# Kernel optimization log

Hardware: AMD Instinct MI355X
Metric: run time of the kernel (lower is better)

Reference implementation:

```python
import jax, jax.numpy as jnp
import numpy as np

B, C, H, W = 512, 1, 280, 280
K, S, F = 28, 28, 10           # kernel, stride, nfilters
HS, WS = 10, 10                # output spatial spans (280/28)
SPAN = HS * WS                 # 100 patch locations
OUT = 10                       # out_channels
DEC_IN = HS * WS * F           # 1000


def setup_inputs() -> dict:
    key = jax.random.key(0)
    k1, k2, k3, k4, k5 = jax.random.split(key, 5)
    x = jax.random.normal(k1, (B, C, H, W), dtype=jnp.float32)
    # locally-connected weights: one kernel per (filter, spatial location), torch layout [F*SPAN, C, K, K]
    conv_w = jax.random.normal(k2, (F * SPAN, C, K, K), dtype=jnp.float32) * 0.02
    conv_b = jax.random.normal(k3, (F * SPAN, C), dtype=jnp.float32) * 0.02
    dec_w = jax.random.normal(k4, (OUT, DEC_IN), dtype=jnp.float32) * 0.02
    dec_b = jax.random.normal(k5, (OUT,), dtype=jnp.float32) * 0.02
    return {"x": x, "conv_w": conv_w, "conv_b": conv_b, "dec_w": dec_w, "dec_b": dec_b}


def reference(x, conv_w, conv_b, dec_w, dec_b):
    # Extract non-overlapping KxK patches (stride == kernel_size, padding == 0):
    # [B,C,H,W] -> [B,C,HS,K,WS,K] -> [B,HS,WS,C,K,K] -> [B,SPAN,C,K,K]
    # matches torch unfold(2).unfold(3) ordering (height span outer, width span inner).
    patches = x.reshape(B, C, HS, K, WS, K).transpose(0, 2, 4, 1, 3, 5)
    patches = patches.reshape(B, SPAN, C, K, K)
    # weight index in torch is f*SPAN + s (x is tiled SPAN-fastest by repeat)
    w = conv_w.reshape(F, SPAN, C, K, K)
    # per-location elementwise mul + reduce over (kh, kw) == batched tiny contraction
    out = jnp.einsum('bscij,fscij->bfsc', patches, w)  # [B,F,SPAN,C]
    out = out + conv_b.reshape(F, SPAN, C)
    out = out.reshape(B, F, HS, WS)  # valid since C == 1 (as in torch view)
    out = jax.nn.relu(out).reshape(B, DEC_IN)
    return out @ dec_w.T + dec_b
```

## Files before the change

### kernel.cpp

```cpp
#include <hip/hip_runtime.h>

#define HW      280
#define IMG     78400
#define KK      28
#define F_N     10
#define SPAN    100
#define OUT_N   10
#define NB      4
#define RQR     14
#define WQ      (RQR * 7)
#define P_PLANE 512000

__device__ __forceinline__ float red8(float v) {
  v += __int_as_float(__builtin_amdgcn_mov_dpp(__float_as_int(v), 0xB1, 0xF, 0xF, true));
  v += __int_as_float(__builtin_amdgcn_mov_dpp(__float_as_int(v), 0x4E, 0xF, 0xF, true));
  v += __int_as_float(__builtin_amdgcn_ds_swizzle(__float_as_int(v), 0x101F));
  return v;
}

__global__ __launch_bounds__(256) void lcn_conv(
    const float* __restrict__ x, const float* __restrict__ cw,
    float* __restrict__ P) {
  const int bid = blockIdx.x;
  const int t   = bid & 7;
  const int s   = bid >> 3;
  const int rq  = t >> 2;
  const int bg  = t & 3;
  const int hs  = s / 10, ws = s - hs * 10;

  const int lane = threadIdx.x & 63;
  const int wid  = threadIdx.x >> 6;
  const int c4   = lane & 7;
  const int g    = lane >> 3;
  const int b0   = bg * 128 + wid * 32 + g * 4;

  __shared__ float4 wl[F_N * WQ];
  {
    const float4* wg = reinterpret_cast<const float4*>(cw);
    for (int i = (int)threadIdx.x; i < F_N * WQ; i += 256) {
      const int f = i / WQ, rem = i - f * WQ;
      wl[i] = wg[(f * SPAN + s) * 196 + rq * WQ + rem];
    }
  }
  __syncthreads();

  float acc[NB][F_N];
#pragma unroll
  for (int bi = 0; bi < NB; ++bi)
#pragma unroll
    for (int f = 0; f < F_N; ++f) acc[bi][f] = 0.f;

  const float* xb = x + (size_t)(hs * KK + rq * RQR) * HW + ws * KK + c4 * 4;
  const float* xr[NB];
#pragma unroll
  for (int bi = 0; bi < NB; ++bi) xr[bi] = xb + (size_t)(b0 + bi) * IMG;

#define COMPUTE(ROW, XV)                                                  \
  {                                                                       \
    _Pragma("unroll")                                                     \
    for (int f = 0; f < F_N; ++f) {                                       \
      const float4 wv = wl[f * WQ + (ROW) * 7 + c4];                      \
      _Pragma("unroll")                                                   \
      for (int bi = 0; bi < NB; ++bi) {                                   \
        acc[bi][f] = fmaf(XV[bi].x, wv.x, acc[bi][f]);                    \
        acc[bi][f] = fmaf(XV[bi].y, wv.y, acc[bi][f]);                    \
        acc[bi][f] = fmaf(XV[bi].z, wv.z, acc[bi][f]);                    \
        acc[bi][f] = fmaf(XV[bi].w, wv.w, acc[bi][f]);                    \
      }                                                                   \
    }                                                                     \
  }

  if (c4 < 7) {
    float4 xvA[NB], xvB[NB];
#pragma unroll
    for (int bi = 0; bi < NB; ++bi)
      xvA[bi] = *reinterpret_cast<const float4*>(xr[bi]);
    for (int r = 0; r < RQR; r += 2) {
#pragma unroll
      for (int bi = 0; bi < NB; ++bi)
        xvB[bi] = *reinterpret_cast<const float4*>(xr[bi] + (size_t)(r + 1) * HW);
      COMPUTE(r, xvA)
      if (r + 2 < RQR) {
#pragma unroll
        for (int bi = 0; bi < NB; ++bi)
          xvA[bi] = *reinterpret_cast<const float4*>(xr[bi] + (size_t)(r + 2) * HW);
      }
      COMPUTE(r + 1, xvB)
    }
  }

#pragma unroll
  for (int bi = 0; bi < NB; ++bi)
#pragma unroll
    for (int f = 0; f < F_N; ++f) acc[bi][f] = red8(acc[bi][f]);

  float* Pp = P + (size_t)rq * P_PLANE + (size_t)s * 512 + b0;
#pragma unroll
  for (int f = 0; f < F_N; ++f) {
    if (c4 == f || c4 == f - 8) {
#pragma unroll
      for (int bi = 0; bi < NB; ++bi)
        Pp[(size_t)f * (SPAN * 512) + bi] = acc[bi][f];
    }
  }
}

__global__ __launch_bounds__(256) void lcn_dec(
    const float* __restrict__ P, const float* __restrict__ cb,
    const float* __restrict__ dw, float* __restrict__ yp) {
  const int bid    = blockIdx.x;
  const int dchunk = bid >> 3;
  const int bg     = bid & 7;
  const int lane   = threadIdx.x & 63;
  const int swid   = __builtin_amdgcn_readfirstlane((int)(threadIdx.x >> 6));
  const int d0     = dchunk * 40 + swid * 10;

  const float* Pb = P + (size_t)bg * 64 + lane;
  float acc[OUT_N];
#pragma unroll
  for (int o = 0; o < OUT_N; ++o) acc[o] = 0.f;

#pragma unroll
  for (int dd = 0; dd < 10; ++dd) {
    const int d = d0 + dd;
    const float p = Pb[(size_t)d * 512] + Pb[(size_t)d * 512 + P_PLANE];
    const float h = fmaxf(p + cb[d], 0.f);
#pragma unroll
    for (int o = 0; o < OUT_N; ++o)
      acc[o] = fmaf(h, dw[o * 1000 + d], acc[o]);
  }
  float* ypp = yp + (size_t)(dchunk * 4 + swid) * 5120 + bg * 64 + lane;
#pragma unroll
  for (int o = 0; o < OUT_N; ++o) ypp[(size_t)o * 512] = acc[o];
}

__global__ __launch_bounds__(256) void lcn_yred(
    const float* __restrict__ yp, const float* __restrict__ db,
    float* __restrict__ y) {
  const int idx = blockIdx.x * 256 + (int)threadIdx.x;
  const int o = idx >> 9;
  const int b = idx & 511;
  float a = db[o];
#pragma unroll 10
  for (int p = 0; p < 100; ++p) a += yp[(size_t)p * 5120 + idx];
  y[b * OUT_N + o] = a;
}

extern "C" void kernel_launch(void* const* d_in, const int* in_sizes, int n_in,
                              void* d_out, int out_size, void* d_ws, size_t ws_size,
                              hipStream_t stream) {
  const float* x  = (const float*)d_in[0];
  const float* cw = (const float*)d_in[1];
  const float* cb = (const float*)d_in[2];
  const float* dw = (const float*)d_in[3];
  const float* db = (const float*)d_in[4];
  float* y = (float*)d_out;

  float* P  = (float*)d_ws;
  float* yp = P + 2 * P_PLANE;

  lcn_conv<<<dim3(800), dim3(256), 0, stream>>>(x, cw, P);
  lcn_dec <<<dim3(200), dim3(256), 0, stream>>>(P, cb, dw, yp);
  lcn_yred<<<dim3(20),  dim3(256), 0, stream>>>(yp, db, y);
}
```

Baseline: 46.84 us.

## Split conv rows into quarters with XCD-aware block mapping and triple-buffered loads

```diff
diff --git a/kernel.cpp b/kernel.cpp
--- a/kernel.cpp
+++ b/kernel.cpp
@@ -7,26 +7,30 @@
 #define SPAN    100
 #define OUT_N   10
 #define NB      4
-#define RQR     14
+#define RQR     7
 #define WQ      (RQR * 7)
 #define P_PLANE 512000
 
 __device__ __forceinline__ float red8(float v) {
-  v += __int_as_float(__builtin_amdgcn_mov_dpp(__float_as_int(v), 0xB1, 0xF, 0xF, true));
-  v += __int_as_float(__builtin_amdgcn_mov_dpp(__float_as_int(v), 0x4E, 0xF, 0xF, true));
-  v += __int_as_float(__builtin_amdgcn_ds_swizzle(__float_as_int(v), 0x101F));
+  v += __int_as_float(__builtin_amdgcn_mov_dpp(__float_as_int(v), 0xB1,  0xF, 0xF, true));
+  v += __int_as_float(__builtin_amdgcn_mov_dpp(__float_as_int(v), 0x4E,  0xF, 0xF, true));
+  v += __int_as_float(__builtin_amdgcn_mov_dpp(__float_as_int(v), 0x141, 0xF, 0xF, true));
   return v;
 }
 
-__global__ __launch_bounds__(256) void lcn_conv(
+__global__ __launch_bounds__(256, 4) void lcn_conv(
     const float* __restrict__ x, const float* __restrict__ cw,
     float* __restrict__ P) {
   const int bid = blockIdx.x;
-  const int t   = bid & 7;
-  const int s   = bid >> 3;
+  const int xcd = bid & 7;
+  const int idx = bid >> 3;
+  const int ws  = idx % 10;
+  const int u   = xcd * 20 + idx / 10;
+  const int hs  = u % 10;
+  const int t   = u / 10;
   const int rq  = t >> 2;
   const int bg  = t & 3;
-  const int hs  = s / 10, ws = s - hs * 10;
+  const int s   = hs * 10 + ws;
 
   const int lane = threadIdx.x & 63;
   const int wid  = threadIdx.x >> 6;
@@ -51,41 +55,37 @@
     for (int f = 0; f < F_N; ++f) acc[bi][f] = 0.f;
 
   const float* xb = x + (size_t)(hs * KK + rq * RQR) * HW + ws * KK + c4 * 4;
-  const float* xr[NB];
-#pragma unroll
-  for (int bi = 0; bi < NB; ++bi) xr[bi] = xb + (size_t)(b0 + bi) * IMG;
 
-#define COMPUTE(ROW, XV)                                                  \
+#define LOADROW(SLOT, ROW)                                                \
+  _Pragma("unroll")                                                       \
+  for (int bi = 0; bi < NB; ++bi)                                         \
+    xv[SLOT][bi] = *reinterpret_cast<const float4*>(                      \
+        xb + (size_t)(b0 + bi) * IMG + (size_t)(ROW) * HW);
+
+#define COMPUTE(ROW, SLOT)                                                \
   {                                                                       \
     _Pragma("unroll")                                                     \
     for (int f = 0; f < F_N; ++f) {                                       \
       const float4 wv = wl[f * WQ + (ROW) * 7 + c4];                      \
       _Pragma("unroll")                                                   \
       for (int bi = 0; bi < NB; ++bi) {                                   \
-        acc[bi][f] = fmaf(XV[bi].x, wv.x, acc[bi][f]);                    \
-        acc[bi][f] = fmaf(XV[bi].y, wv.y, acc[bi][f]);                    \
-        acc[bi][f] = fmaf(XV[bi].z, wv.z, acc[bi][f]);                    \
-        acc[bi][f] = fmaf(XV[bi].w, wv.w, acc[bi][f]);                    \
+        acc[bi][f] = fmaf(xv[SLOT][bi].x, wv.x, acc[bi][f]);              \
+        acc[bi][f] = fmaf(xv[SLOT][bi].y, wv.y, acc[bi][f]);              \
+        acc[bi][f] = fmaf(xv[SLOT][bi].z, wv.z, acc[bi][f]);              \
+        acc[bi][f] = fmaf(xv[SLOT][bi].w, wv.w, acc[bi][f]);              \
       }                                                                   \
     }                                                                     \
   }
 
   if (c4 < 7) {
-    float4 xvA[NB], xvB[NB];
+    float4 xv[3][NB];
+    LOADROW(0, 0)
+    LOADROW(1, 1)
 #pragma unroll
-    for (int bi = 0; bi < NB; ++bi)
-      xvA[bi] = *reinterpret_cast<const float4*>(xr[bi]);
-    for (int r = 0; r < RQR; r += 2) {
-#pragma unroll
-      for (int bi = 0; bi < NB; ++bi)
-        xvB[bi] = *reinterpret_cast<const float4*>(xr[bi] + (size_t)(r + 1) * HW);
-      COMPUTE(r, xvA)
-      if (r + 2 < RQR) {
-#pragma unroll
-        for (int bi = 0; bi < NB; ++bi)
-          xvA[bi] = *reinterpret_cast<const float4*>(xr[bi] + (size_t)(r + 2) * HW);
-      }
-      COMPUTE(r + 1, xvB)
+    for (int r = 0; r < RQR; ++r) {
+      const int slot = r % 3;
+      if (r + 2 < RQR) { const int ns = (r + 2) % 3; LOADROW(ns, r + 2) }
+      COMPUTE(r, slot)
     }
   }
 
@@ -98,9 +98,8 @@
 #pragma unroll
   for (int f = 0; f < F_N; ++f) {
     if (c4 == f || c4 == f - 8) {
-#pragma unroll
-      for (int bi = 0; bi < NB; ++bi)
-        Pp[(size_t)f * (SPAN * 512) + bi] = acc[bi][f];
+      float4 v4 = make_float4(acc[0][f], acc[1][f], acc[2][f], acc[3][f]);
+      *reinterpret_cast<float4*>(&Pp[(size_t)f * (SPAN * 512)]) = v4;
     }
   }
 }
@@ -123,7 +122,8 @@
 #pragma unroll
   for (int dd = 0; dd < 10; ++dd) {
     const int d = d0 + dd;
-    const float p = Pb[(size_t)d * 512] + Pb[(size_t)d * 512 + P_PLANE];
+    const float* pd = Pb + (size_t)d * 512;
+    const float p = pd[0] + pd[P_PLANE] + pd[2 * (size_t)P_PLANE] + pd[3 * (size_t)P_PLANE];
     const float h = fmaxf(p + cb[d], 0.f);
 #pragma unroll
     for (int o = 0; o < OUT_N; ++o)
@@ -157,9 +157,9 @@
   float* y = (float*)d_out;
 
   float* P  = (float*)d_ws;
-  float* yp = P + 2 * P_PLANE;
+  float* yp = P + 4 * (size_t)P_PLANE;
 
-  lcn_conv<<<dim3(800), dim3(256), 0, stream>>>(x, cw, P);
-  lcn_dec <<<dim3(200), dim3(256), 0, stream>>>(P, cb, dw, yp);
-  lcn_yred<<<dim3(20),  dim3(256), 0, stream>>>(yp, db, y);
+  lcn_conv<<<dim3(1600), dim3(256), 0, stream>>>(x, cw, P);
+  lcn_dec <<<dim3(200),  dim3(256), 0, stream>>>(P, cb, dw, yp);
+  lcn_yred<<<dim3(20),   dim3(256), 0, stream>>>(yp, db, y);
 }
```

New measurement: 45.56 us. -2.7%, faster.
